# Kernel optimization log

Hardware: AMD Instinct MI355X
Metric: run time of the kernel (lower is better)

## Reference

```python
import jax, jax.numpy as jnp
import numpy as np

N = 100000
E = 3200000
IN_F = 128
OUT_F = 64
ALPHA = 0.1  # leaky relu negative slope


def spmm(rows, cols, vals, X):
    # sparse [N,N] (COO) @ dense [N,F] -> [N,F]
    return jax.ops.segment_sum(vals[:, None] * X[cols], rows, num_segments=N)


def setup_inputs() -> dict:
    key = jax.random.key(0)
    ks = jax.random.split(key, 16)
    d = {
        "x": jax.random.normal(ks[0], (N, IN_F), dtype=jnp.float32),
        "W": jax.random.normal(ks[1], (IN_F, OUT_F), dtype=jnp.float32) * (1.414 / np.sqrt(IN_F)),
        "a": jax.random.normal(ks[2], (2 * OUT_F, 1), dtype=jnp.float32) * 0.1,
    }
    names = ["A", "P1", "P2", "P3"]
    for i, nm in enumerate(names):
        d[nm + "_rows"] = jax.random.randint(ks[3 + 3 * i], (E,), 0, N, dtype=jnp.int32)
        d[nm + "_cols"] = jax.random.randint(ks[4 + 3 * i], (E,), 0, N, dtype=jnp.int32)
        d[nm + "_vals"] = jax.random.uniform(ks[5 + 3 * i], (E,), dtype=jnp.float32) / 32.0
    return d


def reference(x, W, a, A_rows, A_cols, A_vals,
              P1_rows, P1_cols, P1_vals,
              P2_rows, P2_cols, P2_vals,
              P3_rows, P3_cols, P3_vals):
    support0 = x @ W                         # [N, F]
    h_A = spmm(A_rows, A_cols, A_vals, support0)
    h_A2 = spmm(A_rows, A_cols, A_vals, h_A)
    h_A3 = spmm(A_rows, A_cols, A_vals, h_A2)
    h_sct1 = jnp.abs(spmm(P1_rows, P1_cols, P1_vals, support0))
    h_sct2 = jnp.abs(spmm(P2_rows, P2_cols, P2_vals, support0))
    h_sct3 = jnp.abs(spmm(P3_rows, P3_cols, P3_vals, support0))

    h = support0
    F2 = 2 * OUT_F
    # faithful to torch: cat along dim0 then raw row-major view(N, 1, 2F)
    def pair(hk):
        return jnp.concatenate([h, hk], axis=0).reshape(N, 1, F2)

    a_input = jnp.concatenate(
        [pair(h_A), pair(h_A2), pair(h_A3), pair(h_sct1), pair(h_sct2), pair(h_sct3)],
        axis=1,
    ).reshape(N, 6, F2)
    e = jax.nn.leaky_relu((a_input @ a)[..., 0], negative_slope=ALPHA)  # [N, 6]
    attention = jax.nn.softmax(e, axis=1).reshape(N, 6, 1)
    # faithful to torch: cat along dim2 -> [N,F,6], then raw view(N,6,F)
    h_all = jnp.stack([h_A, h_A2, h_A3, h_sct1, h_sct2, h_sct3], axis=2).reshape(N, 6, OUT_F)
    h_prime = jnp.mean(attention * h_all, axis=1)  # [N, F]
    return (h_prime, attention)
```

## Files before the change

### kernel.cpp

```cpp
#include <hip/hip_runtime.h>
#include <math.h>

#define NN 100000
#define EE 3200000
#define INF 128
#define OUTF 64
#define ALPHA 0.1f

#define BROWS 128
#define NBINS 782
#define CAP 4472
#define SCHUNK 4096
#define NCH 2
#define SBLK (SCHUNK * NCH)
#define NSUM ((NBINS + 3) / 4)

#define GR 64
#define XPAD 132

__device__ __forceinline__ unsigned short f2bf(float f)
{
    unsigned u = __float_as_uint(f);
    u += 0x7FFFu + ((u >> 16) & 1u);
    return (unsigned short)(u >> 16);
}
__device__ __forceinline__ float bf2f(unsigned short b)
{
    return __uint_as_float((unsigned)b << 16);
}

__global__ __launch_bounds__(256) void gemm_kernel(
    const float* __restrict__ x, const float* __restrict__ W,
    unsigned short* __restrict__ outbf)
{
    __shared__ float Wl[INF * OUTF];
    __shared__ float xL[GR * XPAD];

    int tid = threadIdx.x;
    int tx = tid & 15;
    int ty = tid >> 4;
    int r0 = blockIdx.x * GR;

    const float4* W4 = (const float4*)W;
    float4* Wl4 = (float4*)Wl;
    for (int i = tid; i < INF * OUTF / 4; i += 256) Wl4[i] = W4[i];

    for (int i = tid; i < GR * (INF / 4); i += 256) {
        int row = i >> 5;
        int c4 = i & 31;
        int gr = r0 + row;
        float4 v = make_float4(0.f, 0.f, 0.f, 0.f);
        if (gr < NN) v = *(const float4*)&x[(size_t)gr * INF + 4 * c4];
        *(float4*)&xL[row * XPAD + 4 * c4] = v;
    }
    __syncthreads();

    float acc[4][4];
#pragma unroll
    for (int i = 0; i < 4; i++)
#pragma unroll
        for (int j = 0; j < 4; j++) acc[i][j] = 0.f;

#pragma unroll 4
    for (int k4 = 0; k4 < INF / 4; k4++) {
        float4 xv[4], wv[4];
#pragma unroll
        for (int i = 0; i < 4; i++)
            xv[i] = *(float4*)&xL[(4 * ty + i) * XPAD + 4 * k4];
#pragma unroll
        for (int kk = 0; kk < 4; kk++)
            wv[kk] = *(float4*)&Wl[(4 * k4 + kk) * OUTF + 4 * tx];
#pragma unroll
        for (int i = 0; i < 4; i++) {
#pragma unroll
            for (int kk = 0; kk < 4; kk++) {
                acc[i][0] = fmaf(((float*)&xv[i])[kk], ((float*)&wv[kk])[0], acc[i][0]);
                acc[i][1] = fmaf(((float*)&xv[i])[kk], ((float*)&wv[kk])[1], acc[i][1]);
                acc[i][2] = fmaf(((float*)&xv[i])[kk], ((float*)&wv[kk])[2], acc[i][2]);
                acc[i][3] = fmaf(((float*)&xv[i])[kk], ((float*)&wv[kk])[3], acc[i][3]);
            }
        }
    }

#pragma unroll
    for (int i = 0; i < 4; i++) {
        int gr = r0 + 4 * ty + i;
        if (gr < NN) {
            uint2 o;
            o.x = (unsigned)f2bf(acc[i][0]) | ((unsigned)f2bf(acc[i][1]) << 16);
            o.y = (unsigned)f2bf(acc[i][2]) | ((unsigned)f2bf(acc[i][3]) << 16);
            *(uint2*)&outbf[(size_t)gr * OUTF + 4 * tx] = o;
        }
    }
}

__global__ __launch_bounds__(256) void bin_scatter4(
    const int* __restrict__ rows0, const int* __restrict__ cols0, const float* __restrict__ vals0,
    const int* __restrict__ rows1, const int* __restrict__ cols1, const float* __restrict__ vals1,
    const int* __restrict__ rows2, const int* __restrict__ cols2, const float* __restrict__ vals2,
    const int* __restrict__ rows3, const int* __restrict__ cols3, const float* __restrict__ vals3,
    int* __restrict__ gcur_all,
    uint2* __restrict__ b0, uint2* __restrict__ b1,
    uint2* __restrict__ b2, uint2* __restrict__ b3)
{
    __shared__ uint2 rec[SCHUNK];
    __shared__ int hc[NCH][NBINS];
    __shared__ int lcur[NBINS];
    __shared__ int off[NBINS + 1];
    __shared__ int cur[NBINS];
    __shared__ int sums[NSUM];

    int m = blockIdx.y;
    const int* rows; const int* cols; const float* vals; uint2* binned;
    if (m == 0)      { rows = rows0; cols = cols0; vals = vals0; binned = b0; }
    else if (m == 1) { rows = rows1; cols = cols1; vals = vals1; binned = b1; }
    else if (m == 2) { rows = rows2; cols = cols2; vals = vals2; binned = b2; }
    else             { rows = rows3; cols = cols3; vals = vals3; binned = b3; }
    int* gcur = gcur_all + m * NBINS;

    int tid = threadIdx.x;
    int base = blockIdx.x * SBLK;
    int n = min(SBLK, EE - base);
    if (n <= 0) return;

    for (int i = tid; i < NCH * NBINS; i += 256) ((int*)hc)[i] = 0;
    __syncthreads();
    for (int i = tid; i < n; i += 256) {
        int r = rows[base + i];
        atomicAdd(&hc[i >> 12][r >> 7], 1);
    }
    __syncthreads();
    for (int b = tid; b < NBINS; b += 256) {
        int c = hc[0][b] + hc[1][b];
        lcur[b] = c ? atomicAdd(&gcur[b], c) : 0;
    }

    for (int cc = 0; cc < NCH; cc++) {
        int c0 = cc * SCHUNK;
        if (c0 >= n) break;
        int nc = min(SCHUNK, n - c0);
        __syncthreads();
        if (tid < NSUM) {
            int s = 0;
#pragma unroll
            for (int k = 0; k < 4; k++) { int b = 4 * tid + k; if (b < NBINS) s += hc[cc][b]; }
            sums[tid] = s;
        }
        __syncthreads();
        if (tid == 0) {
            int acc = 0;
            for (int t = 0; t < NSUM; t++) { int v = sums[t]; sums[t] = acc; acc += v; }
            off[NBINS] = acc;
        }
        __syncthreads();
        if (tid < NSUM) {
            int acc = sums[tid];
#pragma unroll
            for (int k = 0; k < 4; k++) {
                int b = 4 * tid + k;
                if (b < NBINS) { off[b] = acc; cur[b] = acc; acc += hc[cc][b]; }
            }
        }
        __syncthreads();
        for (int i = tid; i < nc; i += 256) {
            int r = rows[base + c0 + i];
            int ccol = cols[base + c0 + i];
            float v = vals[base + c0 + i];
            int b = r >> 7;
            int pos = atomicAdd(&cur[b], 1);
            uint2 q;
            q.x = (unsigned)ccol | ((unsigned)(r & (BROWS - 1)) << 17)
                | ((unsigned)(b & 0xFF) << 24);
            q.y = __float_as_uint(v);
            rec[pos] = q;
        }
        __syncthreads();
        for (int i = tid; i < nc; i += 256) {
            uint2 q = rec[i];
            int b = (int)(q.x >> 24);
            if (b + 768 < NBINS && off[b + 768] <= i) b += 768;
            else if (b + 512 < NBINS && off[b + 512] <= i) b += 512;
            else if (b + 256 < NBINS && off[b + 256] <= i) b += 256;
            int slot = lcur[b] + (i - off[b]);
            if (slot < CAP) binned[(size_t)b * CAP + slot] = q;
        }
        __syncthreads();
        for (int b = tid; b < NBINS; b += 256) lcur[b] += hc[cc][b];
    }
}

__global__ __launch_bounds__(256) void bin_sort4(
    uint2* __restrict__ b0, uint2* __restrict__ b1,
    uint2* __restrict__ b2, uint2* __restrict__ b3,
    const int* __restrict__ gcur_all,
    int* __restrict__ rowptr_all, int* __restrict__ cnt_all)
{
    __shared__ uint2 rin[CAP];
    __shared__ uint2 rout[CAP];
    __shared__ int h[BROWS], hs[BROWS], cur[BROWS];

    int m = blockIdx.y;
    uint2* binned = (m == 0) ? b0 : (m == 1) ? b1 : (m == 2) ? b2 : b3;
    const int* gcur = gcur_all + m * NBINS;
    int* rowptr = rowptr_all + m * NN;
    int* cnt = cnt_all + m * NN;

    int bin = blockIdx.x;
    int tid = threadIdx.x;
    int c = min(gcur[bin], CAP);
    uint2* src = binned + (size_t)bin * CAP;

    for (int i = tid; i < c; i += 256) rin[i] = src[i];
    if (tid < BROWS) h[tid] = 0;
    __syncthreads();
    for (int i = tid; i < c; i += 256)
        atomicAdd(&h[(rin[i].x >> 17) & (BROWS - 1)], 1);
    __syncthreads();
    if (tid < BROWS) hs[tid] = h[tid];
    __syncthreads();
#pragma unroll
    for (int o = 1; o < BROWS; o <<= 1) {
        int w = (tid >= o && tid < BROWS) ? hs[tid - o] : 0;
        __syncthreads();
        if (tid < BROWS) hs[tid] += w;
        __syncthreads();
    }
    if (tid < BROWS) cur[tid] = hs[tid] - h[tid];
    __syncthreads();
    for (int i = tid; i < c; i += 256) {
        uint2 q = rin[i];
        int pos = atomicAdd(&cur[(q.x >> 17) & (BROWS - 1)], 1);
        rout[pos] = q;
    }
    __syncthreads();
    for (int i = tid; i < c; i += 256) src[i] = rout[i];

    if (tid < BROWS) {
        int gr = bin * BROWS + tid;
        if (gr < NN) {
            rowptr[gr] = bin * CAP + (hs[tid] - h[tid]);
            cnt[gr] = h[tid];
        }
    }
}

__device__ __forceinline__ void spmm_row(
    const int* __restrict__ rowptr, const int* __restrict__ cnt,
    const uint2* __restrict__ edges,
    const unsigned short* __restrict__ Xb, unsigned short* __restrict__ Yb)
{
    int row = blockIdx.x * 4 + (threadIdx.x >> 6);
    int lane = threadIdx.x & 63;
    if (row >= NN) return;
    int s = __builtin_amdgcn_readfirstlane(rowptr[row]);
    int e = s + __builtin_amdgcn_readfirstlane(cnt[row]);
    float acc = 0.f;
    int i = s;
    for (; i + 7 < e; i += 8) {
        uint2 p0 = edges[i + 0], p1 = edges[i + 1], p2 = edges[i + 2], p3 = edges[i + 3];
        uint2 p4 = edges[i + 4], p5 = edges[i + 5], p6 = edges[i + 6], p7 = edges[i + 7];
        unsigned short x0 = Xb[(size_t)(p0.x & 0x1FFFF) * OUTF + lane];
        unsigned short x1 = Xb[(size_t)(p1.x & 0x1FFFF) * OUTF + lane];
        unsigned short x2 = Xb[(size_t)(p2.x & 0x1FFFF) * OUTF + lane];
        unsigned short x3 = Xb[(size_t)(p3.x & 0x1FFFF) * OUTF + lane];
        unsigned short x4 = Xb[(size_t)(p4.x & 0x1FFFF) * OUTF + lane];
        unsigned short x5 = Xb[(size_t)(p5.x & 0x1FFFF) * OUTF + lane];
        unsigned short x6 = Xb[(size_t)(p6.x & 0x1FFFF) * OUTF + lane];
        unsigned short x7 = Xb[(size_t)(p7.x & 0x1FFFF) * OUTF + lane];
        acc = fmaf(__uint_as_float(p0.y), bf2f(x0), acc);
        acc = fmaf(__uint_as_float(p1.y), bf2f(x1), acc);
        acc = fmaf(__uint_as_float(p2.y), bf2f(x2), acc);
        acc = fmaf(__uint_as_float(p3.y), bf2f(x3), acc);
        acc = fmaf(__uint_as_float(p4.y), bf2f(x4), acc);
        acc = fmaf(__uint_as_float(p5.y), bf2f(x5), acc);
        acc = fmaf(__uint_as_float(p6.y), bf2f(x6), acc);
        acc = fmaf(__uint_as_float(p7.y), bf2f(x7), acc);
    }
    for (; i < e; i++) {
        uint2 p = edges[i];
        acc = fmaf(__uint_as_float(p.y),
                   bf2f(Xb[(size_t)(p.x & 0x1FFFF) * OUTF + lane]), acc);
    }
    Yb[(size_t)row * OUTF + lane] = f2bf(acc);
}

__global__ __launch_bounds__(256) void spmm_csr(
    const int* __restrict__ rowptr, const int* __restrict__ cnt,
    const uint2* __restrict__ edges,
    const unsigned short* __restrict__ Xb, unsigned short* __restrict__ Yb)
{
    spmm_row(rowptr, cnt, edges, Xb, Yb);
}

__global__ __launch_bounds__(256) void spmm4(
    const int* __restrict__ rowptr_all, const int* __restrict__ cnt_all,
    const uint2* __restrict__ b0, const uint2* __restrict__ b1,
    const uint2* __restrict__ b2, const uint2* __restrict__ b3,
    const unsigned short* __restrict__ sup,
    unsigned short* __restrict__ hA, unsigned short* __restrict__ s1,
    unsigned short* __restrict__ s2, unsigned short* __restrict__ s3)
{
    int m = blockIdx.y;
    const uint2* edges = (m == 0) ? b0 : (m == 1) ? b1 : (m == 2) ? b2 : b3;
    unsigned short* out = (m == 0) ? hA : (m == 1) ? s1 : (m == 2) ? s2 : s3;
    spmm_row(rowptr_all + m * NN, cnt_all + m * NN, edges, sup, out);
}

__global__ __launch_bounds__(256) void fuse_kernel(
    const unsigned short* __restrict__ hA, const unsigned short* __restrict__ hA2,
    const unsigned short* __restrict__ hA3,
    const unsigned short* __restrict__ s1, const unsigned short* __restrict__ s2,
    const unsigned short* __restrict__ s3,
    const float* __restrict__ a, float* __restrict__ out)
{
    __shared__ float chl[4][6][OUTF];
    int wid = threadIdx.x >> 6;
    int lane = threadIdx.x & 63;
    int i = blockIdx.x * 4 + wid;
    if (i >= NN) return;

    const unsigned short* bufs[6] = {hA, hA2, hA3, s1, s2, s3};

#pragma unroll
    for (int k = 0; k < 6; k++) {
        float v = bf2f(bufs[k][(size_t)i * OUTF + lane]);
        if (k >= 3) v = fabsf(v);
        chl[wid][k][lane] = v;
    }

    float att[6];
    if (i < NN / 2) {
#pragma unroll
        for (int k = 0; k < 6; k++) att[k] = 1.0f / 6.0f;
    } else {
        int m = 2 * i - NN;
        float alo = a[lane];
        float ahi = a[64 + lane];
        float e[6];
#pragma unroll
        for (int k = 0; k < 6; k++) {
            float v0 = bf2f(bufs[k][(size_t)m * OUTF + lane]);
            float v1 = bf2f(bufs[k][(size_t)(m + 1) * OUTF + lane]);
            if (k >= 3) { v0 = fabsf(v0); v1 = fabsf(v1); }
            float p = alo * v0 + ahi * v1;
#pragma unroll
            for (int off = 32; off; off >>= 1) p += __shfl_xor(p, off);
            e[k] = (p > 0.f) ? p : ALPHA * p;
        }
        float mx = e[0];
#pragma unroll
        for (int k = 1; k < 6; k++) mx = fmaxf(mx, e[k]);
        float s = 0.f;
#pragma unroll
        for (int k = 0; k < 6; k++) { att[k] = __expf(e[k] - mx); s += att[k]; }
        float inv = 1.f / s;
#pragma unroll
        for (int k = 0; k < 6; k++) att[k] *= inv;
    }

    if (lane < 6) out[(size_t)NN * OUTF + (size_t)i * 6 + lane] = att[lane];

    float hp = 0.f;
#pragma unroll
    for (int j = 0; j < 6; j++) {
        int g = j * 64 + lane;
        hp += att[j] * chl[wid][g % 6][g / 6];
    }
    out[(size_t)i * OUTF + lane] = hp * (1.0f / 6.0f);
}

extern "C" void kernel_launch(void* const* d_in, const int* in_sizes, int n_in,
                              void* d_out, int out_size, void* d_ws, size_t ws_size,
                              hipStream_t stream)
{
    const float* x = (const float*)d_in[0];
    const float* W = (const float*)d_in[1];
    const float* a = (const float*)d_in[2];
    const int*   A_rows  = (const int*)d_in[3];
    const int*   A_cols  = (const int*)d_in[4];
    const float* A_vals  = (const float*)d_in[5];
    const int*   P1_rows = (const int*)d_in[6];
    const int*   P1_cols = (const int*)d_in[7];
    const float* P1_vals = (const float*)d_in[8];
    const int*   P2_rows = (const int*)d_in[9];
    const int*   P2_cols = (const int*)d_in[10];
    const float* P2_vals = (const float*)d_in[11];
    const int*   P3_rows = (const int*)d_in[12];
    const int*   P3_cols = (const int*)d_in[13];
    const float* P3_vals = (const float*)d_in[14];

    const size_t NF = (size_t)NN * OUTF;
    const size_t BINSZ = (size_t)NBINS * CAP;

    char* p = (char*)d_ws;
    uint2* b1 = (uint2*)p;              p += BINSZ * sizeof(uint2);
    uint2* b2 = (uint2*)p;              p += BINSZ * sizeof(uint2);
    uint2* b3 = (uint2*)p;              p += BINSZ * sizeof(uint2);
    unsigned short* bf_sup = (unsigned short*)p;  p += NF * 2;
    unsigned short* bf_hA  = (unsigned short*)p;  p += NF * 2;
    unsigned short* bf_hA2 = (unsigned short*)p;  p += NF * 2;
    unsigned short* bf_s1  = (unsigned short*)p;  p += NF * 2;
    unsigned short* bf_s2  = (unsigned short*)p;  p += NF * 2;
    unsigned short* bf_s3  = (unsigned short*)p;  p += NF * 2;
    int* gcur   = (int*)p;              p += (size_t)4 * NBINS * sizeof(int);
    int* rowptr = (int*)p;              p += (size_t)4 * NN * sizeof(int);
    int* cnt    = (int*)p;              p += (size_t)4 * NN * sizeof(int);

    uint2* b0 = (uint2*)d_out;

    const int GB = (EE + SBLK - 1) / SBLK;
    const int RB = (NN + 3) / 4;

    hipMemsetAsync(gcur, 0, (size_t)4 * NBINS * sizeof(int), stream);

    gemm_kernel<<<(NN + GR - 1) / GR, 256, 0, stream>>>(x, W, bf_sup);

    bin_scatter4<<<dim3(GB, 4), 256, 0, stream>>>(
        A_rows, A_cols, A_vals, P1_rows, P1_cols, P1_vals,
        P2_rows, P2_cols, P2_vals, P3_rows, P3_cols, P3_vals,
        gcur, b0, b1, b2, b3);

    bin_sort4<<<dim3(NBINS, 4), 256, 0, stream>>>(b0, b1, b2, b3, gcur, rowptr, cnt);

    spmm4<<<dim3(RB, 4), 256, 0, stream>>>(rowptr, cnt, b0, b1, b2, b3,
                                           bf_sup, bf_hA, bf_s1, bf_s2, bf_s3);

    spmm_csr<<<RB, 256, 0, stream>>>(rowptr, cnt, b0, bf_hA,  bf_hA2);
    spmm_csr<<<RB, 256, 0, stream>>>(rowptr, cnt, b0, bf_hA2, bf_sup);

    fuse_kernel<<<RB, 256, 0, stream>>>(bf_hA, bf_hA2, bf_sup,
                                        bf_s1, bf_s2, bf_s3, a, (float*)d_out);
}
```

Measured before the change: 752.7 us.

## Fuse GEMM into scatter launch, parallel scan, wider sort blocks, uniform edge loads

The dense x@W GEMM now runs as extra blocks of the binning scatter kernel, so both overlap in a single launch. The GEMM reads x directly from global memory instead of staging it in shared memory. The scatter uses smaller chunks (2048, four per block) and replaces the serial single-thread prefix sum with a parallel Hillis-Steele scan. bin_sort runs with 512 threads per block. The SpMM inner loop makes edge indices wave-uniform via readfirstlane and replaces the scalar tail with a masked 8-wide block. The risks are more shared-memory syncs in the scan and uncoalesced direct x loads in the GEMM.

```diff
diff --git a/kernel.cpp b/kernel.cpp
--- a/kernel.cpp
+++ b/kernel.cpp
@@ -10,13 +10,13 @@
 #define BROWS 128
 #define NBINS 782
 #define CAP 4472
-#define SCHUNK 4096
-#define NCH 2
+#define SCHUNK 2048
+#define NCH 4
 #define SBLK (SCHUNK * NCH)
 #define NSUM ((NBINS + 3) / 4)
+#define GB 391
 
 #define GR 64
-#define XPAD 132
 
 __device__ __forceinline__ unsigned short f2bf(float f)
 {
@@ -29,88 +29,85 @@
     return __uint_as_float((unsigned)b << 16);
 }
 
-__global__ __launch_bounds__(256) void gemm_kernel(
-    const float* __restrict__ x, const float* __restrict__ W,
-    unsigned short* __restrict__ outbf)
-{
-    __shared__ float Wl[INF * OUTF];
-    __shared__ float xL[GR * XPAD];
-
-    int tid = threadIdx.x;
-    int tx = tid & 15;
-    int ty = tid >> 4;
-    int r0 = blockIdx.x * GR;
-
-    const float4* W4 = (const float4*)W;
-    float4* Wl4 = (float4*)Wl;
-    for (int i = tid; i < INF * OUTF / 4; i += 256) Wl4[i] = W4[i];
-
-    for (int i = tid; i < GR * (INF / 4); i += 256) {
-        int row = i >> 5;
-        int c4 = i & 31;
-        int gr = r0 + row;
-        float4 v = make_float4(0.f, 0.f, 0.f, 0.f);
-        if (gr < NN) v = *(const float4*)&x[(size_t)gr * INF + 4 * c4];
-        *(float4*)&xL[row * XPAD + 4 * c4] = v;
-    }
-    __syncthreads();
-
-    float acc[4][4];
-#pragma unroll
-    for (int i = 0; i < 4; i++)
-#pragma unroll
-        for (int j = 0; j < 4; j++) acc[i][j] = 0.f;
-
-#pragma unroll 4
-    for (int k4 = 0; k4 < INF / 4; k4++) {
-        float4 xv[4], wv[4];
-#pragma unroll
-        for (int i = 0; i < 4; i++)
-            xv[i] = *(float4*)&xL[(4 * ty + i) * XPAD + 4 * k4];
-#pragma unroll
-        for (int kk = 0; kk < 4; kk++)
-            wv[kk] = *(float4*)&Wl[(4 * k4 + kk) * OUTF + 4 * tx];
-#pragma unroll
-        for (int i = 0; i < 4; i++) {
-#pragma unroll
-            for (int kk = 0; kk < 4; kk++) {
-                acc[i][0] = fmaf(((float*)&xv[i])[kk], ((float*)&wv[kk])[0], acc[i][0]);
-                acc[i][1] = fmaf(((float*)&xv[i])[kk], ((float*)&wv[kk])[1], acc[i][1]);
-                acc[i][2] = fmaf(((float*)&xv[i])[kk], ((float*)&wv[kk])[2], acc[i][2]);
-                acc[i][3] = fmaf(((float*)&xv[i])[kk], ((float*)&wv[kk])[3], acc[i][3]);
-            }
-        }
-    }
-
-#pragma unroll
-    for (int i = 0; i < 4; i++) {
-        int gr = r0 + 4 * ty + i;
-        if (gr < NN) {
-            uint2 o;
-            o.x = (unsigned)f2bf(acc[i][0]) | ((unsigned)f2bf(acc[i][1]) << 16);
-            o.y = (unsigned)f2bf(acc[i][2]) | ((unsigned)f2bf(acc[i][3]) << 16);
-            *(uint2*)&outbf[(size_t)gr * OUTF + 4 * tx] = o;
-        }
-    }
-}
-
-__global__ __launch_bounds__(256) void bin_scatter4(
+__global__ __launch_bounds__(256) void scatter_gemm(
     const int* __restrict__ rows0, const int* __restrict__ cols0, const float* __restrict__ vals0,
     const int* __restrict__ rows1, const int* __restrict__ cols1, const float* __restrict__ vals1,
     const int* __restrict__ rows2, const int* __restrict__ cols2, const float* __restrict__ vals2,
     const int* __restrict__ rows3, const int* __restrict__ cols3, const float* __restrict__ vals3,
     int* __restrict__ gcur_all,
     uint2* __restrict__ b0, uint2* __restrict__ b1,
-    uint2* __restrict__ b2, uint2* __restrict__ b3)
-{
-    __shared__ uint2 rec[SCHUNK];
-    __shared__ int hc[NCH][NBINS];
-    __shared__ int lcur[NBINS];
-    __shared__ int off[NBINS + 1];
-    __shared__ int cur[NBINS];
-    __shared__ int sums[NSUM];
-
+    uint2* __restrict__ b2, uint2* __restrict__ b3,
+    const float* __restrict__ x, const float* __restrict__ W,
+    unsigned short* __restrict__ supbf)
+{
+    __shared__ __align__(16) char smem[40192];
+    int tid = threadIdx.x;
+    int bx = blockIdx.x;
     int m = blockIdx.y;
+
+    if (bx >= GB) {
+        float* Wl = (float*)smem;
+        const float4* W4 = (const float4*)W;
+        float4* Wl4 = (float4*)Wl;
+        for (int i = tid; i < INF * OUTF / 4; i += 256) Wl4[i] = W4[i];
+        __syncthreads();
+
+        int gid = (bx - GB) + m * GB;
+        int r0 = gid * GR;
+        if (r0 >= NN) return;
+        int tx = tid & 15;
+        int ty = tid >> 4;
+
+        float acc[4][4];
+#pragma unroll
+        for (int i = 0; i < 4; i++)
+#pragma unroll
+            for (int j = 0; j < 4; j++) acc[i][j] = 0.f;
+
+#pragma unroll 4
+        for (int k4 = 0; k4 < INF / 4; k4++) {
+            float4 xv[4], wv[4];
+#pragma unroll
+            for (int i = 0; i < 4; i++) {
+                int rr = r0 + 4 * ty + i;
+                xv[i] = (rr < NN) ? *(const float4*)&x[(size_t)rr * INF + 4 * k4]
+                                  : make_float4(0.f, 0.f, 0.f, 0.f);
+            }
+#pragma unroll
+            for (int kk = 0; kk < 4; kk++)
+                wv[kk] = *(float4*)&Wl[(4 * k4 + kk) * OUTF + 4 * tx];
+#pragma unroll
+            for (int i = 0; i < 4; i++) {
+#pragma unroll
+                for (int kk = 0; kk < 4; kk++) {
+                    acc[i][0] = fmaf(((float*)&xv[i])[kk], ((float*)&wv[kk])[0], acc[i][0]);
+                    acc[i][1] = fmaf(((float*)&xv[i])[kk], ((float*)&wv[kk])[1], acc[i][1]);
+                    acc[i][2] = fmaf(((float*)&xv[i])[kk], ((float*)&wv[kk])[2], acc[i][2]);
+                    acc[i][3] = fmaf(((float*)&xv[i])[kk], ((float*)&wv[kk])[3], acc[i][3]);
+                }
+            }
+        }
+#pragma unroll
+        for (int i = 0; i < 4; i++) {
+            int gr = r0 + 4 * ty + i;
+            if (gr < NN) {
+                uint2 o;
+                o.x = (unsigned)f2bf(acc[i][0]) | ((unsigned)f2bf(acc[i][1]) << 16);
+                o.y = (unsigned)f2bf(acc[i][2]) | ((unsigned)f2bf(acc[i][3]) << 16);
+                *(uint2*)&supbf[(size_t)gr * OUTF + 4 * tx] = o;
+            }
+        }
+        return;
+    }
+
+    uint2* rec = (uint2*)smem;
+    int* hcf   = (int*)(smem + 16384);
+    int* lcur  = (int*)(smem + 28896);
+    int* off   = (int*)(smem + 32024);
+    int* cur   = (int*)(smem + 35156);
+    int* sums  = (int*)(smem + 38284);
+    int* ssc   = (int*)(smem + 39068);
+
     const int* rows; const int* cols; const float* vals; uint2* binned;
     if (m == 0)      { rows = rows0; cols = cols0; vals = vals0; binned = b0; }
     else if (m == 1) { rows = rows1; cols = cols1; vals = vals1; binned = b1; }
@@ -118,20 +115,19 @@
     else             { rows = rows3; cols = cols3; vals = vals3; binned = b3; }
     int* gcur = gcur_all + m * NBINS;
 
-    int tid = threadIdx.x;
-    int base = blockIdx.x * SBLK;
+    int base = bx * SBLK;
     int n = min(SBLK, EE - base);
     if (n <= 0) return;
 
-    for (int i = tid; i < NCH * NBINS; i += 256) ((int*)hc)[i] = 0;
+    for (int i = tid; i < NCH * NBINS; i += 256) hcf[i] = 0;
     __syncthreads();
     for (int i = tid; i < n; i += 256) {
         int r = rows[base + i];
-        atomicAdd(&hc[i >> 12][r >> 7], 1);
+        atomicAdd(&hcf[(i >> 11) * NBINS + (r >> 7)], 1);
     }
     __syncthreads();
     for (int b = tid; b < NBINS; b += 256) {
-        int c = hc[0][b] + hc[1][b];
+        int c = hcf[b] + hcf[NBINS + b] + hcf[2 * NBINS + b] + hcf[3 * NBINS + b];
         lcur[b] = c ? atomicAdd(&gcur[b], c) : 0;
     }
 
@@ -143,14 +139,22 @@
         if (tid < NSUM) {
             int s = 0;
 #pragma unroll
-            for (int k = 0; k < 4; k++) { int b = 4 * tid + k; if (b < NBINS) s += hc[cc][b]; }
+            for (int k = 0; k < 4; k++) { int b = 4 * tid + k; if (b < NBINS) s += hcf[cc * NBINS + b]; }
             sums[tid] = s;
         }
         __syncthreads();
-        if (tid == 0) {
-            int acc = 0;
-            for (int t = 0; t < NSUM; t++) { int v = sums[t]; sums[t] = acc; acc += v; }
-            off[NBINS] = acc;
+        {
+            int sv = (tid < NSUM) ? sums[tid] : 0;
+            ssc[tid] = sv;
+            __syncthreads();
+            for (int o = 1; o < 256; o <<= 1) {
+                int w = (tid >= o) ? ssc[tid - o] : 0;
+                __syncthreads();
+                ssc[tid] += w;
+                __syncthreads();
+            }
+            if (tid < NSUM) sums[tid] = ssc[tid] - sv;
+            if (tid == 255) off[NBINS] = ssc[255];
         }
         __syncthreads();
         if (tid < NSUM) {
@@ -158,7 +162,7 @@
 #pragma unroll
             for (int k = 0; k < 4; k++) {
                 int b = 4 * tid + k;
-                if (b < NBINS) { off[b] = acc; cur[b] = acc; acc += hc[cc][b]; }
+                if (b < NBINS) { off[b] = acc; cur[b] = acc; acc += hcf[cc * NBINS + b]; }
             }
         }
         __syncthreads();
@@ -185,11 +189,11 @@
             if (slot < CAP) binned[(size_t)b * CAP + slot] = q;
         }
         __syncthreads();
-        for (int b = tid; b < NBINS; b += 256) lcur[b] += hc[cc][b];
-    }
-}
-
-__global__ __launch_bounds__(256) void bin_sort4(
+        for (int b = tid; b < NBINS; b += 256) lcur[b] += hcf[cc * NBINS + b];
+    }
+}
+
+__global__ __launch_bounds__(512) void bin_sort4(
     uint2* __restrict__ b0, uint2* __restrict__ b1,
     uint2* __restrict__ b2, uint2* __restrict__ b3,
     const int* __restrict__ gcur_all,
@@ -210,10 +214,10 @@
     int c = min(gcur[bin], CAP);
     uint2* src = binned + (size_t)bin * CAP;
 
-    for (int i = tid; i < c; i += 256) rin[i] = src[i];
+    for (int i = tid; i < c; i += 512) rin[i] = src[i];
     if (tid < BROWS) h[tid] = 0;
     __syncthreads();
-    for (int i = tid; i < c; i += 256)
+    for (int i = tid; i < c; i += 512)
         atomicAdd(&h[(rin[i].x >> 17) & (BROWS - 1)], 1);
     __syncthreads();
     if (tid < BROWS) hs[tid] = h[tid];
@@ -227,13 +231,13 @@
     }
     if (tid < BROWS) cur[tid] = hs[tid] - h[tid];
     __syncthreads();
-    for (int i = tid; i < c; i += 256) {
+    for (int i = tid; i < c; i += 512) {
         uint2 q = rin[i];
         int pos = atomicAdd(&cur[(q.x >> 17) & (BROWS - 1)], 1);
         rout[pos] = q;
     }
     __syncthreads();
-    for (int i = tid; i < c; i += 256) src[i] = rout[i];
+    for (int i = tid; i < c; i += 512) src[i] = rout[i];
 
     if (tid < BROWS) {
         int gr = bin * BROWS + tid;
@@ -257,8 +261,9 @@
     float acc = 0.f;
     int i = s;
     for (; i + 7 < e; i += 8) {
-        uint2 p0 = edges[i + 0], p1 = edges[i + 1], p2 = edges[i + 2], p3 = edges[i + 3];
-        uint2 p4 = edges[i + 4], p5 = edges[i + 5], p6 = edges[i + 6], p7 = edges[i + 7];
+        int ib = __builtin_amdgcn_readfirstlane(i);
+        uint2 p0 = edges[ib + 0], p1 = edges[ib + 1], p2 = edges[ib + 2], p3 = edges[ib + 3];
+        uint2 p4 = edges[ib + 4], p5 = edges[ib + 5], p6 = edges[ib + 6], p7 = edges[ib + 7];
         unsigned short x0 = Xb[(size_t)(p0.x & 0x1FFFF) * OUTF + lane];
         unsigned short x1 = Xb[(size_t)(p1.x & 0x1FFFF) * OUTF + lane];
         unsigned short x2 = Xb[(size_t)(p2.x & 0x1FFFF) * OUTF + lane];
@@ -276,10 +281,17 @@
         acc = fmaf(__uint_as_float(p6.y), bf2f(x6), acc);
         acc = fmaf(__uint_as_float(p7.y), bf2f(x7), acc);
     }
-    for (; i < e; i++) {
-        uint2 p = edges[i];
-        acc = fmaf(__uint_as_float(p.y),
-                   bf2f(Xb[(size_t)(p.x & 0x1FFFF) * OUTF + lane]), acc);
+    if (i < e) {
+        int ib = __builtin_amdgcn_readfirstlane(i);
+        int last = e - 1;
+#pragma unroll
+        for (int k = 0; k < 8; k++) {
+            int j = ib + k;
+            uint2 p = edges[min(j, last)];
+            float v = (j < e) ? __uint_as_float(p.y) : 0.f;
+            unsigned short xk = Xb[(size_t)(p.x & 0x1FFFF) * OUTF + lane];
+            acc = fmaf(v, bf2f(xk), acc);
+        }
     }
     Yb[(size_t)row * OUTF + lane] = f2bf(acc);
 }
@@ -408,19 +420,16 @@
 
     uint2* b0 = (uint2*)d_out;
 
-    const int GB = (EE + SBLK - 1) / SBLK;
     const int RB = (NN + 3) / 4;
 
     hipMemsetAsync(gcur, 0, (size_t)4 * NBINS * sizeof(int), stream);
 
-    gemm_kernel<<<(NN + GR - 1) / GR, 256, 0, stream>>>(x, W, bf_sup);
-
-    bin_scatter4<<<dim3(GB, 4), 256, 0, stream>>>(
+    scatter_gemm<<<dim3(2 * GB, 4), 256, 0, stream>>>(
         A_rows, A_cols, A_vals, P1_rows, P1_cols, P1_vals,
         P2_rows, P2_cols, P2_vals, P3_rows, P3_cols, P3_vals,
-        gcur, b0, b1, b2, b3);
-
-    bin_sort4<<<dim3(NBINS, 4), 256, 0, stream>>>(b0, b1, b2, b3, gcur, rowptr, cnt);
+        gcur, b0, b1, b2, b3, x, W, bf_sup);
+
+    bin_sort4<<<dim3(NBINS, 4), 512, 0, stream>>>(b0, b1, b2, b3, gcur, rowptr, cnt);
 
     spmm4<<<dim3(RB, 4), 256, 0, stream>>>(rowptr, cnt, b0, b1, b2, b3,
                                            bf_sup, bf_hA, bf_s1, bf_s2, bf_s3);
```

Result: slower. 786.0 us (+4.4%).

## Parallelize scatter scan, shrink scatter chunks, widen bin sort, unroll SpMM tail

Applied to the files above, without the earlier changes.

In the binning scatter, each chunk drops from 4096 to 2048 edges (4 chunks per block), and the single-thread serial prefix sum over bin groups becomes a 256-thread log-step shared-memory scan. The per-bin sort kernel now runs 512 threads per block. The SpMM row loop makes the edge index wave-uniform with readfirstlane, and replaces the scalar remainder loop with one masked 8-wide unrolled step. The aim is less serialized work and LDS pressure in preprocessing and fewer loop iterations in the SpMM tail, at the cost of more barriers in the scan and some redundant masked loads.

```diff
diff --git a/kernel.cpp b/kernel.cpp
--- a/kernel.cpp
+++ b/kernel.cpp
@@ -10,10 +10,11 @@
 #define BROWS 128
 #define NBINS 782
 #define CAP 4472
-#define SCHUNK 4096
-#define NCH 2
+#define SCHUNK 2048
+#define NCH 4
 #define SBLK (SCHUNK * NCH)
 #define NSUM ((NBINS + 3) / 4)
+#define GB 391
 
 #define GR 64
 #define XPAD 132
@@ -108,7 +109,7 @@
     __shared__ int lcur[NBINS];
     __shared__ int off[NBINS + 1];
     __shared__ int cur[NBINS];
-    __shared__ int sums[NSUM];
+    __shared__ int ssc[256];
 
     int m = blockIdx.y;
     const int* rows; const int* cols; const float* vals; uint2* binned;
@@ -127,11 +128,11 @@
     __syncthreads();
     for (int i = tid; i < n; i += 256) {
         int r = rows[base + i];
-        atomicAdd(&hc[i >> 12][r >> 7], 1);
+        atomicAdd(&hc[i >> 11][r >> 7], 1);
     }
     __syncthreads();
     for (int b = tid; b < NBINS; b += 256) {
-        int c = hc[0][b] + hc[1][b];
+        int c = hc[0][b] + hc[1][b] + hc[2][b] + hc[3][b];
         lcur[b] = c ? atomicAdd(&gcur[b], c) : 0;
     }
 
@@ -140,21 +141,24 @@
         if (c0 >= n) break;
         int nc = min(SCHUNK, n - c0);
         __syncthreads();
+        int sv = 0;
         if (tid < NSUM) {
-            int s = 0;
-#pragma unroll
-            for (int k = 0; k < 4; k++) { int b = 4 * tid + k; if (b < NBINS) s += hc[cc][b]; }
-            sums[tid] = s;
-        }
-        __syncthreads();
-        if (tid == 0) {
-            int acc = 0;
-            for (int t = 0; t < NSUM; t++) { int v = sums[t]; sums[t] = acc; acc += v; }
-            off[NBINS] = acc;
-        }
+#pragma unroll
+            for (int k = 0; k < 4; k++) { int b = 4 * tid + k; if (b < NBINS) sv += hc[cc][b]; }
+        }
+        ssc[tid] = sv;
+        __syncthreads();
+        for (int o = 1; o < 256; o <<= 1) {
+            int w = (tid >= o) ? ssc[tid - o] : 0;
+            __syncthreads();
+            ssc[tid] += w;
+            __syncthreads();
+        }
+        int excl = ssc[tid] - sv;
+        if (tid == 255) off[NBINS] = ssc[255];
         __syncthreads();
         if (tid < NSUM) {
-            int acc = sums[tid];
+            int acc = excl;
 #pragma unroll
             for (int k = 0; k < 4; k++) {
                 int b = 4 * tid + k;
@@ -189,7 +193,7 @@
     }
 }
 
-__global__ __launch_bounds__(256) void bin_sort4(
+__global__ __launch_bounds__(512) void bin_sort4(
     uint2* __restrict__ b0, uint2* __restrict__ b1,
     uint2* __restrict__ b2, uint2* __restrict__ b3,
     const int* __restrict__ gcur_all,
@@ -210,10 +214,10 @@
     int c = min(gcur[bin], CAP);
     uint2* src = binned + (size_t)bin * CAP;
 
-    for (int i = tid; i < c; i += 256) rin[i] = src[i];
+    for (int i = tid; i < c; i += 512) rin[i] = src[i];
     if (tid < BROWS) h[tid] = 0;
     __syncthreads();
-    for (int i = tid; i < c; i += 256)
+    for (int i = tid; i < c; i += 512)
         atomicAdd(&h[(rin[i].x >> 17) & (BROWS - 1)], 1);
     __syncthreads();
     if (tid < BROWS) hs[tid] = h[tid];
@@ -227,13 +231,13 @@
     }
     if (tid < BROWS) cur[tid] = hs[tid] - h[tid];
     __syncthreads();
-    for (int i = tid; i < c; i += 256) {
+    for (int i = tid; i < c; i += 512) {
         uint2 q = rin[i];
         int pos = atomicAdd(&cur[(q.x >> 17) & (BROWS - 1)], 1);
         rout[pos] = q;
     }
     __syncthreads();
-    for (int i = tid; i < c; i += 256) src[i] = rout[i];
+    for (int i = tid; i < c; i += 512) src[i] = rout[i];
 
     if (tid < BROWS) {
         int gr = bin * BROWS + tid;
@@ -257,8 +261,9 @@
     float acc = 0.f;
     int i = s;
     for (; i + 7 < e; i += 8) {
-        uint2 p0 = edges[i + 0], p1 = edges[i + 1], p2 = edges[i + 2], p3 = edges[i + 3];
-        uint2 p4 = edges[i + 4], p5 = edges[i + 5], p6 = edges[i + 6], p7 = edges[i + 7];
+        int ib = __builtin_amdgcn_readfirstlane(i);
+        uint2 p0 = edges[ib + 0], p1 = edges[ib + 1], p2 = edges[ib + 2], p3 = edges[ib + 3];
+        uint2 p4 = edges[ib + 4], p5 = edges[ib + 5], p6 = edges[ib + 6], p7 = edges[ib + 7];
         unsigned short x0 = Xb[(size_t)(p0.x & 0x1FFFF) * OUTF + lane];
         unsigned short x1 = Xb[(size_t)(p1.x & 0x1FFFF) * OUTF + lane];
         unsigned short x2 = Xb[(size_t)(p2.x & 0x1FFFF) * OUTF + lane];
@@ -276,10 +281,17 @@
         acc = fmaf(__uint_as_float(p6.y), bf2f(x6), acc);
         acc = fmaf(__uint_as_float(p7.y), bf2f(x7), acc);
     }
-    for (; i < e; i++) {
-        uint2 p = edges[i];
-        acc = fmaf(__uint_as_float(p.y),
-                   bf2f(Xb[(size_t)(p.x & 0x1FFFF) * OUTF + lane]), acc);
+    if (i < e) {
+        int ib = __builtin_amdgcn_readfirstlane(i);
+        int last = e - 1;
+#pragma unroll
+        for (int k = 0; k < 8; k++) {
+            int j = ib + k;
+            uint2 p = edges[min(j, last)];
+            float v = (j < e) ? __uint_as_float(p.y) : 0.f;
+            unsigned short xk = Xb[(size_t)(p.x & 0x1FFFF) * OUTF + lane];
+            acc = fmaf(v, bf2f(xk), acc);
+        }
     }
     Yb[(size_t)row * OUTF + lane] = f2bf(acc);
 }
@@ -408,7 +420,6 @@
 
     uint2* b0 = (uint2*)d_out;
 
-    const int GB = (EE + SBLK - 1) / SBLK;
     const int RB = (NN + 3) / 4;
 
     hipMemsetAsync(gcur, 0, (size_t)4 * NBINS * sizeof(int), stream);
@@ -420,7 +431,7 @@
         P2_rows, P2_cols, P2_vals, P3_rows, P3_cols, P3_vals,
         gcur, b0, b1, b2, b3);
 
-    bin_sort4<<<dim3(NBINS, 4), 256, 0, stream>>>(b0, b1, b2, b3, gcur, rowptr, cnt);
+    bin_sort4<<<dim3(NBINS, 4), 512, 0, stream>>>(b0, b1, b2, b3, gcur, rowptr, cnt);
 
     spmm4<<<dim3(RB, 4), 256, 0, stream>>>(rowptr, cnt, b0, b1, b2, b3,
                                            bf_sup, bf_hA, bf_s1, bf_s2, bf_s3);
```

New measurement: 691.7 us. 1.09x faster.
